# Kernel tuning notes

Measured on AMD Instinct MI355X. Metric: run time of the kernel, lower is better.

## Reference

```python
import jax, jax.numpy as jnp
import numpy as np

B, T, C, HD = 4, 4096, 1024, 64

def setup_inputs() -> dict:
    key = jax.random.key(0)
    k1, k2, k3, k4 = jax.random.split(key, 4)
    x = jax.random.normal(k1, (B, T, C), dtype=jnp.float32)
    scale = 1.0 / np.sqrt(C)
    Wq = jax.random.normal(k2, (C, HD), dtype=jnp.float32) * scale
    Wk = jax.random.normal(k3, (C, HD), dtype=jnp.float32) * scale
    Wv = jax.random.normal(k4, (C, HD), dtype=jnp.float32) * scale
    return {"x": x, "Wq": Wq, "Wk": Wk, "Wv": Wv}

def reference(x, Wq, Wk, Wv):
    # q,k,v: [B,T,HD]
    q = jnp.einsum('btc,ch->bth', x, Wq)
    k = jnp.einsum('btc,ch->bth', x, Wk)
    v = jnp.einsum('btc,ch->bth', x, Wv)
    hd = q.shape[-1]
    scores = jnp.einsum('bth,bsh->bts', q, k) / jnp.sqrt(jnp.float32(hd))  # [B,T,T]
    causal = jnp.tril(jnp.ones((scores.shape[1], scores.shape[1]), dtype=bool))
    scores = jnp.where(causal, scores, -jnp.inf)
    attn = jax.nn.softmax(scores, axis=-1)
    return jnp.einsum('bts,bsh->bth', attn, v)  # [B,T,HD]
```

## Files before the change

### kernel.cpp

```cpp
#include <hip/hip_runtime.h>
#include <hip/hip_bf16.h>

typedef __attribute__((ext_vector_type(8))) short bf16x8;
typedef __attribute__((ext_vector_type(4))) short bf16x4;
typedef __attribute__((ext_vector_type(4))) float f32x4;
typedef __attribute__((ext_vector_type(4))) int   i32x4;

#define C2LOG 0.18033688011112042f
#define THR_RAW 44.3616f

__device__ __forceinline__ short f2bf(float f) {
    union { float f; unsigned u; } v; v.f = f;
    unsigned r = v.u + 0x7fff + ((v.u >> 16) & 1);
    return (short)(r >> 16);
}
__device__ __forceinline__ unsigned cvtpk(float lo, float hi) {
    unsigned r;
    asm("v_cvt_pk_bf16_f32 %0, %1, %2" : "=v"(r) : "v"(lo), "v"(hi));
    return r;
}
__device__ __forceinline__ float bf2f(short s) {
    union { unsigned u; float f; } v; v.u = ((unsigned)(unsigned short)s) << 16;
    return v.f;
}
__device__ __forceinline__ float4 gload4(const float* p) {
    float4 r;
    asm volatile("global_load_dwordx4 %0, %1, off"
                 : "=&v"(r) : "v"(p) : "memory");
    return r;
}

#define BB 4
#define TT 4096
#define CC 1024
#define HD 64
#define NTASK_PB 144
#define NTASK (BB * NTASK_PB)

__global__ __launch_bounds__(256) void prep_w(const float* __restrict__ Wq,
        const float* __restrict__ Wk, const float* __restrict__ Wv,
        short* __restrict__ Wt) {
    __shared__ float wls[64][65];
    const int w = blockIdx.x >> 4;
    const int c = blockIdx.x & 15;
    const float* W = (w == 0) ? Wq : (w == 1) ? Wk : Wv;

    const int r  = threadIdx.x >> 4;
    const int q4 = threadIdx.x & 15;
    #pragma unroll
    for (int rr = 0; rr < 4; ++rr) {
        const int row = rr * 16 + r;
        float4 v = *reinterpret_cast<const float4*>(
            W + (size_t)(c * 64 + row) * HD + q4 * 4);
        wls[row][q4 * 4 + 0] = v.x;
        wls[row][q4 * 4 + 1] = v.y;
        wls[row][q4 * 4 + 2] = v.z;
        wls[row][q4 * 4 + 3] = v.w;
    }
    __syncthreads();

    const int n  = threadIdx.x >> 2;
    const int ks = (threadIdx.x & 3) * 16;
    bf16x8 o0, o1;
    #pragma unroll
    for (int j = 0; j < 8; ++j) o0[j] = f2bf(wls[ks + j][n]);
    #pragma unroll
    for (int j = 0; j < 8; ++j) o1[j] = f2bf(wls[ks + 8 + j][n]);
    short* dst = Wt + (size_t)(w * 64 + n) * CC + c * 64 + ks;
    *reinterpret_cast<bf16x8*>(dst)     = o0;
    *reinterpret_cast<bf16x8*>(dst + 8) = o1;
}

__global__ __launch_bounds__(512) void proj_qkv(const float* __restrict__ x,
        const short* __restrict__ Wt, short* __restrict__ Q,
        short* __restrict__ K, short* __restrict__ Vt) {
    __shared__ short xs[2][32 * 72];
    __shared__ short wsm[2][192 * 64];

    const int tid  = threadIdx.x;
    const int lane = tid & 63;
    const int wv   = tid >> 6;
    const int lm   = lane & 15;
    const int lg   = lane >> 4;
    const int mhalf = wv & 1;
    const int ngrp  = wv >> 1;
    const int mbase = blockIdx.x * 32;

    const int xr  = tid >> 4;
    const int xq4 = tid & 15;
    const float* xrow = x + (size_t)(mbase + xr) * CC;

    int wsrow[3], wscol[3];
    #pragma unroll
    for (int it = 0; it < 3; ++it) {
        const int off = it * 8192 + wv * 1024 + lane * 16;
        wsrow[it] = off >> 7;
        wscol[it] = (off & 127) ^ ((wsrow[it] & 7) << 4);
    }

#define STAGE_W(bufidx, kc)                                                           \
    {                                                                                 \
        _Pragma("unroll")                                                             \
        for (int it = 0; it < 3; ++it) {                                              \
            const char* src = (const char*)(Wt + (size_t)wsrow[it] * CC + (kc) * 64)  \
                              + wscol[it];                                            \
            char* dst = (char*)&wsm[bufidx][0] + it * 8192 + wv * 1024;               \
            __builtin_amdgcn_global_load_lds(                                         \
                (const __attribute__((address_space(1))) unsigned*)src,               \
                (__attribute__((address_space(3))) unsigned*)dst, 16, 0, 0);          \
        }                                                                             \
    }

#define CONV_X(bufidx, xv)                                                            \
    {                                                                                 \
        int2 pk;                                                                      \
        pk.x = (int)cvtpk((xv).x, (xv).y);                                            \
        pk.y = (int)cvtpk((xv).z, (xv).w);                                            \
        *reinterpret_cast<int2*>(&xs[bufidx][xr * 72 + xq4 * 4]) = pk;                \
    }

    f32x4 acc[3];
    #pragma unroll
    for (int i = 0; i < 3; ++i) acc[i] = f32x4{0.f, 0.f, 0.f, 0.f};

    {
        float4 v = *reinterpret_cast<const float4*>(xrow + xq4 * 4);
        CONV_X(0, v)
        STAGE_W(0, 0)
    }
    float4 vA = gload4(xrow + 64 + xq4 * 4);
    asm volatile("s_waitcnt vmcnt(1)" ::: "memory");
    asm volatile("s_waitcnt lgkmcnt(0)" ::: "memory");
    __builtin_amdgcn_s_barrier();

    const int arow = mhalf * 16 + lm;
    int buf = 0;
    for (int kc = 0; kc < 16; ++kc) {
        if (kc < 15) STAGE_W(buf ^ 1, kc + 1)
        float4 vB;
        if (kc < 14) vB = gload4(xrow + (kc + 2) * 64 + xq4 * 4);

        bf16x8 a0 = *reinterpret_cast<const bf16x8*>(&xs[buf][arow * 72 + lg * 8]);
        bf16x8 a1 = *reinterpret_cast<const bf16x8*>(&xs[buf][arow * 72 + 32 + lg * 8]);
        __builtin_amdgcn_s_setprio(1);
        #pragma unroll
        for (int c = 0; c < 3; ++c) {
            const int brow = (ngrp * 3 + c) * 16 + lm;
            const int sw = (brow & 7) << 4;
            bf16x8 b0 = *reinterpret_cast<const bf16x8*>(
                (const char*)&wsm[buf][0] + brow * 128 + ((lg * 16) ^ sw));
            bf16x8 b1 = *reinterpret_cast<const bf16x8*>(
                (const char*)&wsm[buf][0] + brow * 128 + ((64 + lg * 16) ^ sw));
            acc[c] = __builtin_amdgcn_mfma_f32_16x16x32_bf16(a0, b0, acc[c], 0, 0, 0);
            acc[c] = __builtin_amdgcn_mfma_f32_16x16x32_bf16(a1, b1, acc[c], 0, 0, 0);
        }
        __builtin_amdgcn_s_setprio(0);

        if (kc < 15) {
            if (kc < 14) asm volatile("s_waitcnt vmcnt(4)" ::: "memory");
            else         asm volatile("s_waitcnt vmcnt(3)" ::: "memory");
            __builtin_amdgcn_sched_barrier(0);
            CONV_X(buf ^ 1, vA)
        }
        vA = vB;

        if (kc < 15) {
            __builtin_amdgcn_sched_barrier(0);
            if (kc < 14) asm volatile("s_waitcnt vmcnt(1)" ::: "memory");
            else         asm volatile("s_waitcnt vmcnt(0)" ::: "memory");
            asm volatile("s_waitcnt lgkmcnt(0)" ::: "memory");
            __builtin_amdgcn_s_barrier();
        }
        buf ^= 1;
    }
#undef STAGE_W
#undef CONV_X

    const int mrow = mbase + mhalf * 16 + lg * 4;
    #pragma unroll
    for (int c = 0; c < 3; ++c) {
        const int cn = ngrp * 3 + c;
        if (cn < 4) {
            #pragma unroll
            for (int r = 0; r < 4; ++r)
                Q[(size_t)(mrow + r) * HD + cn * 16 + lm] = f2bf(acc[c][r]);
        } else if (cn < 8) {
            #pragma unroll
            for (int r = 0; r < 4; ++r)
                K[(size_t)(mrow + r) * HD + (cn - 4) * 16 + lm] = f2bf(acc[c][r]);
        } else {
            const int bb   = mbase >> 12;
            const int tloc = (mbase & 4095) + mhalf * 16 + lg * 4;
            int2 pk;
            pk.x = (int)cvtpk(acc[c][0], acc[c][1]);
            pk.y = (int)cvtpk(acc[c][2], acc[c][3]);
            *reinterpret_cast<int2*>(
                Vt + (size_t)bb * (HD * TT) + (size_t)((cn - 8) * 16 + lm) * TT + tloc) = pk;
        }
    }
}

__global__ __launch_bounds__(256, 3) void attn(const short* __restrict__ Q,
        const short* __restrict__ K, const short* __restrict__ Vt,
        short* __restrict__ Opart, float* __restrict__ Mpart,
        float* __restrict__ Lpart, float* __restrict__ out) {
    __shared__ short ks[3][64 * 64];
    __shared__ short vs[3][64 * 64];

    const int tid  = threadIdx.x;
    const int lane = tid & 63;
    const int wv   = tid >> 6;
    const int lm   = lane & 15;
    const int lg   = lane >> 4;

    const int task = (blockIdx.x & 7) * (NTASK / 8) + (blockIdx.x >> 3);
    const int b  = task / NTASK_PB;
    int t_in = task - b * NTASK_PB;
    int g = 0;
    while (t_in >= 2 * (g + 1) * (g + 2)) ++g;
    const int idx = t_in - 2 * g * (g + 1);
    const int i   = 4 * g + idx / (g + 1);
    const int seg = idx % (g + 1);
    const int S   = g + 1;
    const int niter = 2 * i + 2;
    const int nloop = (niter - seg + S - 1) / S;

    const size_t qkb = (size_t)b * TT * HD;
    const size_t vtb = (size_t)b * HD * TT;
    const int qrow = i * 128 + wv * 32;
    const int tmax = (qrow + 31) >> 6;

    bf16x8 qf0 = *reinterpret_cast<const bf16x8*>(Q + qkb + (size_t)(qrow + lm) * HD + lg * 8);
    bf16x8 qf1 = *reinterpret_cast<const bf16x8*>(Q + qkb + (size_t)(qrow + lm) * HD + 32 + lg * 8);
    bf16x8 qf2 = *reinterpret_cast<const bf16x8*>(Q + qkb + (size_t)(qrow + 16 + lm) * HD + lg * 8);
    bf16x8 qf3 = *reinterpret_cast<const bf16x8*>(Q + qkb + (size_t)(qrow + 16 + lm) * HD + 32 + lg * 8);

    f32x4 oA[4], oB[4];
    #pragma unroll
    for (int c = 0; c < 4; ++c) { oA[c] = f32x4{0.f,0.f,0.f,0.f}; oB[c] = f32x4{0.f,0.f,0.f,0.f}; }
    float mrunA = -1e30f, lrunA = 0.f;
    float mrunB = -1e30f, lrunB = 0.f;

    const int srcA = lm + ((lane & 16) << 1);
    const int srcB = srcA + 16;
    const bool hihalf = (lane & 32) != 0;

    int srow[2], scol[2];
    #pragma unroll
    for (int c = 0; c < 2; ++c) {
        const int off = wv * 2048 + c * 1024 + lane * 16;
        srow[c] = off >> 7;
        scol[c] = (off & 127) ^ ((srow[c] & 7) << 4);
    }

#define STAGE_KV(bufidx, tt)                                                          \
    {                                                                                 \
        _Pragma("unroll")                                                             \
        for (int c = 0; c < 2; ++c) {                                                 \
            const char* ksrc = (const char*)(K + qkb) + (tt) * 8192                   \
                               + (srow[c] << 7) + scol[c];                            \
            char* kdst = (char*)&ks[bufidx][0] + wv * 2048 + c * 1024;                \
            __builtin_amdgcn_global_load_lds(                                         \
                (const __attribute__((address_space(1))) unsigned*)ksrc,              \
                (__attribute__((address_space(3))) unsigned*)kdst, 16, 0, 0);         \
            const char* vsrc = (const char*)(Vt + vtb) + (size_t)srow[c] * (TT * 2)   \
                               + (tt) * 128 + scol[c];                                \
            char* vdst = (char*)&vs[bufidx][0] + wv * 2048 + c * 1024;                \
            __builtin_amdgcn_global_load_lds(                                         \
                (const __attribute__((address_space(1))) unsigned*)vsrc,              \
                (__attribute__((address_space(3))) unsigned*)vdst, 16, 0, 0);         \
        }                                                                             \
    }

    STAGE_KV(0, seg)
    if (nloop > 1) {
        STAGE_KV(1, seg + S)
        asm volatile("s_waitcnt vmcnt(4)" ::: "memory");
    } else {
        asm volatile("s_waitcnt vmcnt(0)" ::: "memory");
    }
    __builtin_amdgcn_s_barrier();

    for (int n = 0; n < nloop; ++n) {
        const int t = seg + n * S;
        const bool stage2 = (n + 2 < nloop);
        if (stage2) STAGE_KV((n + 2) % 3, t + 2 * S)

        if (t <= tmax) {
            const short* ksb = &ks[n % 3][0];
            const short* vsb = &vs[n % 3][0];
            const int kv = t * 64;

            f32x4 stA[4], stB[4];
            __builtin_amdgcn_s_setprio(1);
            #pragma unroll
            for (int kt = 0; kt < 4; ++kt) {
                const int krow = kt * 16 + lm;
                const int sw = (krow & 7) << 4;
                bf16x8 k0 = *reinterpret_cast<const bf16x8*>(
                    (const char*)ksb + krow * 128 + ((lg * 16) ^ sw));
                bf16x8 k1 = *reinterpret_cast<const bf16x8*>(
                    (const char*)ksb + krow * 128 + ((64 + lg * 16) ^ sw));
                f32x4 a = f32x4{0.f,0.f,0.f,0.f};
                a = __builtin_amdgcn_mfma_f32_16x16x32_bf16(k0, qf0, a, 0, 0, 0);
                a = __builtin_amdgcn_mfma_f32_16x16x32_bf16(k1, qf1, a, 0, 0, 0);
                stA[kt] = a;
                f32x4 bb2 = f32x4{0.f,0.f,0.f,0.f};
                bb2 = __builtin_amdgcn_mfma_f32_16x16x32_bf16(k0, qf2, bb2, 0, 0, 0);
                bb2 = __builtin_amdgcn_mfma_f32_16x16x32_bf16(k1, qf3, bb2, 0, 0, 0);
                stB[kt] = bb2;
            }
            __builtin_amdgcn_s_setprio(0);

            if (kv + 63 > qrow) {
                const int qgA = qrow + lm;
                const int qgB = qrow + 16 + lm;
                #pragma unroll
                for (int kt = 0; kt < 4; ++kt)
                    #pragma unroll
                    for (int r = 0; r < 4; ++r) {
                        const int kk = kv + kt * 16 + lg * 4 + r;
                        if (kk > qgA) stA[kt][r] = -1e30f;
                        if (kk > qgB) stB[kt][r] = -1e30f;
                    }
            }

            float mA0 = fmaxf(fmaxf(stA[0][0], stA[0][1]), fmaxf(stA[0][2], stA[0][3]));
            float mA1 = fmaxf(fmaxf(stA[1][0], stA[1][1]), fmaxf(stA[1][2], stA[1][3]));
            float mA2 = fmaxf(fmaxf(stA[2][0], stA[2][1]), fmaxf(stA[2][2], stA[2][3]));
            float mA3 = fmaxf(fmaxf(stA[3][0], stA[3][1]), fmaxf(stA[3][2], stA[3][3]));
            float mlocA = fmaxf(fmaxf(mA0, mA1), fmaxf(mA2, mA3));
            float mB0 = fmaxf(fmaxf(stB[0][0], stB[0][1]), fmaxf(stB[0][2], stB[0][3]));
            float mB1 = fmaxf(fmaxf(stB[1][0], stB[1][1]), fmaxf(stB[1][2], stB[1][3]));
            float mB2 = fmaxf(fmaxf(stB[2][0], stB[2][1]), fmaxf(stB[2][2], stB[2][3]));
            float mB3 = fmaxf(fmaxf(stB[3][0], stB[3][1]), fmaxf(stB[3][2], stB[3][3]));
            float mlocB = fmaxf(fmaxf(mB0, mB1), fmaxf(mB2, mB3));
            mlocA = fmaxf(mlocA, __shfl_xor(mlocA, 16));
            mlocA = fmaxf(mlocA, __shfl_xor(mlocA, 32));
            mlocB = fmaxf(mlocB, __shfl_xor(mlocB, 16));
            mlocB = fmaxf(mlocB, __shfl_xor(mlocB, 32));

            if (!__all(mlocA <= mrunA + THR_RAW)) {
                const float mnewA = fmaxf(mrunA, mlocA);
                const float alphaA = __builtin_amdgcn_exp2f((mrunA - mnewA) * C2LOG);
                mrunA = mnewA;
                lrunA *= alphaA;
                #pragma unroll
                for (int c = 0; c < 4; ++c)
                    #pragma unroll
                    for (int r = 0; r < 4; ++r) oA[c][r] *= alphaA;
            }
            if (!__all(mlocB <= mrunB + THR_RAW)) {
                const float mnewB = fmaxf(mrunB, mlocB);
                const float alphaB = __builtin_amdgcn_exp2f((mrunB - mnewB) * C2LOG);
                mrunB = mnewB;
                lrunB *= alphaB;
                #pragma unroll
                for (int c = 0; c < 4; ++c)
                    #pragma unroll
                    for (int r = 0; r < 4; ++r) oB[c][r] *= alphaB;
            }

            const float ncA = -mrunA * C2LOG;
            const float ncB = -mrunB * C2LOG;
            float pA[4][4], pB[4][4];
            float rsA = 0.f, rsB = 0.f;
            #pragma unroll
            for (int kt = 0; kt < 4; ++kt)
                #pragma unroll
                for (int r = 0; r < 4; ++r) {
                    pA[kt][r] = __builtin_amdgcn_exp2f(__builtin_fmaf(stA[kt][r], C2LOG, ncA));
                    rsA += pA[kt][r];
                    pB[kt][r] = __builtin_amdgcn_exp2f(__builtin_fmaf(stB[kt][r], C2LOG, ncB));
                    rsB += pB[kt][r];
                }
            rsA += __shfl_xor(rsA, 16); rsA += __shfl_xor(rsA, 32);
            rsB += __shfl_xor(rsB, 16); rsB += __shfl_xor(rsB, 32);
            lrunA += rsA;
            lrunB += rsB;

            unsigned uA[4][2], uB[4][2];
            #pragma unroll
            for (int kt = 0; kt < 4; ++kt) {
                uA[kt][0] = cvtpk(pA[kt][0], pA[kt][1]);
                uA[kt][1] = cvtpk(pA[kt][2], pA[kt][3]);
                uB[kt][0] = cvtpk(pB[kt][0], pB[kt][1]);
                uB[kt][1] = cvtpk(pB[kt][2], pB[kt][3]);
            }

            #pragma unroll
            for (int h = 0; h < 2; ++h) {
                const int a0 = __shfl((int)uA[2*h][0],   srcA);
                const int a1c = __shfl((int)uA[2*h+1][0], srcA);
                const int a2 = __shfl((int)uA[2*h][1],   srcA);
                const int a3c = __shfl((int)uA[2*h+1][1], srcA);
                const int a4 = __shfl((int)uA[2*h][0],   srcB);
                const int a5c = __shfl((int)uA[2*h+1][0], srcB);
                const int a6 = __shfl((int)uA[2*h][1],   srcB);
                const int a7c = __shfl((int)uA[2*h+1][1], srcB);
                union { i32x4 iv; bf16x8 v; } cvA;
                cvA.iv = i32x4{ hihalf ? a1c : a0, hihalf ? a3c : a2,
                                hihalf ? a5c : a4, hihalf ? a7c : a6 };
                const int b0 = __shfl((int)uB[2*h][0],   srcA);
                const int b1c = __shfl((int)uB[2*h+1][0], srcA);
                const int b2 = __shfl((int)uB[2*h][1],   srcA);
                const int b3c = __shfl((int)uB[2*h+1][1], srcA);
                const int b4 = __shfl((int)uB[2*h][0],   srcB);
                const int b5c = __shfl((int)uB[2*h+1][0], srcB);
                const int b6 = __shfl((int)uB[2*h][1],   srcB);
                const int b7c = __shfl((int)uB[2*h+1][1], srcB);
                union { i32x4 iv; bf16x8 v; } cvB;
                cvB.iv = i32x4{ hihalf ? b1c : b0, hihalf ? b3c : b2,
                                hihalf ? b5c : b4, hihalf ? b7c : b6 };
                __builtin_amdgcn_s_setprio(1);
                #pragma unroll
                for (int c = 0; c < 4; ++c) {
                    const int vrow = c * 16 + lm;
                    const int sw = (vrow & 7) << 4;
                    bf16x8 va = *reinterpret_cast<const bf16x8*>(
                        (const char*)vsb + vrow * 128 + ((h * 64 + lg * 16) ^ sw));
                    oA[c] = __builtin_amdgcn_mfma_f32_16x16x32_bf16(va, cvA.v, oA[c], 0, 0, 0);
                    oB[c] = __builtin_amdgcn_mfma_f32_16x16x32_bf16(va, cvB.v, oB[c], 0, 0, 0);
                }
                __builtin_amdgcn_s_setprio(0);
            }
        }

        __builtin_amdgcn_sched_barrier(0);
        asm volatile("s_waitcnt lgkmcnt(0)" ::: "memory");
        if (stage2) asm volatile("s_waitcnt vmcnt(4)" ::: "memory");
        else        asm volatile("s_waitcnt vmcnt(0)" ::: "memory");
        __builtin_amdgcn_s_barrier();
    }
#undef STAGE_KV

    if (S == 1) {
        const float invA = 1.0f / lrunA;
        const float invB = 1.0f / lrunB;
        float* Orow = out + ((size_t)b * TT + i * 128) * HD;
        #pragma unroll
        for (int c = 0; c < 4; ++c) {
            f32x4 ra, rb;
            #pragma unroll
            for (int r = 0; r < 4; ++r) { ra[r] = oA[c][r] * invA; rb[r] = oB[c][r] * invB; }
            *reinterpret_cast<f32x4*>(&Orow[(size_t)(wv * 32 + lm) * HD + c * 16 + lg * 4]) = ra;
            *reinterpret_cast<f32x4*>(&Orow[(size_t)(wv * 32 + 16 + lm) * HD + c * 16 + lg * 4]) = rb;
        }
        return;
    }

    short* Ob = Opart + (size_t)task * (128 * HD);
    #pragma unroll
    for (int c = 0; c < 4; ++c) {
        int2 pkA, pkB;
        pkA.x = (int)cvtpk(oA[c][0], oA[c][1]);
        pkA.y = (int)cvtpk(oA[c][2], oA[c][3]);
        pkB.x = (int)cvtpk(oB[c][0], oB[c][1]);
        pkB.y = (int)cvtpk(oB[c][2], oB[c][3]);
        *reinterpret_cast<int2*>(&Ob[(wv * 32 + lm) * HD + c * 16 + lg * 4]) = pkA;
        *reinterpret_cast<int2*>(&Ob[(wv * 32 + 16 + lm) * HD + c * 16 + lg * 4]) = pkB;
    }
    if (lg == 0) {
        Mpart[task * 128 + wv * 32 + lm] = mrunA;
        Lpart[task * 128 + wv * 32 + lm] = lrunA;
        Mpart[task * 128 + wv * 32 + 16 + lm] = mrunB;
        Lpart[task * 128 + wv * 32 + 16 + lm] = lrunB;
    }
}

__global__ __launch_bounds__(256) void combine(const short* __restrict__ Opart,
        const float* __restrict__ Mpart, const float* __restrict__ Lpart,
        float* __restrict__ out) {
    const int b   = blockIdx.x / 224;
    const int rem = blockIdx.x - b * 224;
    const int i   = 4 + (rem >> 3);
    const int rr  = rem & 7;
    const int g = i >> 2;
    const int S = g + 1;
    const int task0 = b * NTASK_PB + 2 * g * (g + 1) + (i - 4 * g) * (g + 1);
    const int qbase = i * 128;

    const int tid = threadIdx.x;
    const int row = rr * 16 + (tid >> 4);
    const int cb  = (tid & 15) << 2;

    float mmax = -1e30f;
    float ms[8];
    for (int s = 0; s < S; ++s) {
        ms[s] = Mpart[(task0 + s) * 128 + row];
        mmax = fmaxf(mmax, ms[s]);
    }
    float lsum = 0.f;
    float a0 = 0.f, a1 = 0.f, a2 = 0.f, a3 = 0.f;
    for (int s = 0; s < S; ++s) {
        const float w = __builtin_amdgcn_exp2f((ms[s] - mmax) * C2LOG);
        lsum += Lpart[(task0 + s) * 128 + row] * w;
        bf16x4 ov = *reinterpret_cast<const bf16x4*>(
            &Opart[((size_t)(task0 + s) * 128 + row) * HD + cb]);
        a0 += bf2f(ov[0]) * w;
        a1 += bf2f(ov[1]) * w;
        a2 += bf2f(ov[2]) * w;
        a3 += bf2f(ov[3]) * w;
    }
    const float inv = 1.0f / lsum;
    f32x4 res{ a0 * inv, a1 * inv, a2 * inv, a3 * inv };
    *reinterpret_cast<f32x4*>(
        &out[((size_t)b * TT + qbase + row) * HD + cb]) = res;
}

extern "C" void kernel_launch(void* const* d_in, const int* in_sizes, int n_in,
                              void* d_out, int out_size, void* d_ws, size_t ws_size,
                              hipStream_t stream) {
    const float* x  = (const float*)d_in[0];
    const float* Wq = (const float*)d_in[1];
    const float* Wk = (const float*)d_in[2];
    const float* Wv = (const float*)d_in[3];
    float* out = (float*)d_out;

    char* ws = (char*)d_ws;
    short* Wt    = (short*)(ws);
    short* Q     = (short*)(ws + 393216);
    short* K     = (short*)(ws + 2490368);
    short* Vt    = (short*)(ws + 4587520);
    short* Opart = (short*)(ws + 6684672);
    float* Mpart = (float*)(ws + 16121856);
    float* Lpart = (float*)(ws + 16416768);

    hipLaunchKernelGGL(prep_w,   dim3(48),    dim3(256), 0, stream, Wq, Wk, Wv, Wt);
    hipLaunchKernelGGL(proj_qkv, dim3(512),   dim3(512), 0, stream, x, Wt, Q, K, Vt);
    hipLaunchKernelGGL(attn,     dim3(NTASK), dim3(256), 0, stream, Q, K, Vt,
                       Opart, Mpart, Lpart, out);
    hipLaunchKernelGGL(combine,  dim3(896),   dim3(256), 0, stream,
                       Opart, Mpart, Lpart, out);
}
```

Baseline: 61.41 us.

## Split attention block into 8 waves with 16 query rows each

The attention kernel now launches 512 threads (8 waves) per block, and each wave handles 16 query rows instead of 32. Every wave stages one 16-byte chunk of K and V per tile instead of two. This halves per-wave register state (accumulators, scores, probabilities), which should raise occupancy and latency hiding. The cost is that each K/V fragment read from LDS now feeds half as many MFMAs, so LDS traffic per FLOP doubles, and barrier synchronization now spans more waves. The launch bound claims 6 blocks of 512 threads, which may not fit on the hardware and could force heavy register limits.

New measurement: 61.47 us. No clear change (+0.1%).

```diff
diff --git a/kernel.cpp b/kernel.cpp
--- a/kernel.cpp
+++ b/kernel.cpp
@@ -200,7 +200,7 @@
     }
 }
 
-__global__ __launch_bounds__(256, 3) void attn(const short* __restrict__ Q,
+__global__ __launch_bounds__(512, 6) void attn(const short* __restrict__ Q,
         const short* __restrict__ K, const short* __restrict__ Vt,
         short* __restrict__ Opart, float* __restrict__ Mpart,
         float* __restrict__ Lpart, float* __restrict__ out) {
@@ -227,55 +227,44 @@
 
     const size_t qkb = (size_t)b * TT * HD;
     const size_t vtb = (size_t)b * HD * TT;
-    const int qrow = i * 128 + wv * 32;
-    const int tmax = (qrow + 31) >> 6;
+    const int qrow = i * 128 + wv * 16;
+    const int tmax = (qrow + 15) >> 6;
 
     bf16x8 qf0 = *reinterpret_cast<const bf16x8*>(Q + qkb + (size_t)(qrow + lm) * HD + lg * 8);
     bf16x8 qf1 = *reinterpret_cast<const bf16x8*>(Q + qkb + (size_t)(qrow + lm) * HD + 32 + lg * 8);
-    bf16x8 qf2 = *reinterpret_cast<const bf16x8*>(Q + qkb + (size_t)(qrow + 16 + lm) * HD + lg * 8);
-    bf16x8 qf3 = *reinterpret_cast<const bf16x8*>(Q + qkb + (size_t)(qrow + 16 + lm) * HD + 32 + lg * 8);
-
-    f32x4 oA[4], oB[4];
-    #pragma unroll
-    for (int c = 0; c < 4; ++c) { oA[c] = f32x4{0.f,0.f,0.f,0.f}; oB[c] = f32x4{0.f,0.f,0.f,0.f}; }
-    float mrunA = -1e30f, lrunA = 0.f;
-    float mrunB = -1e30f, lrunB = 0.f;
+
+    f32x4 o[4];
+    #pragma unroll
+    for (int c = 0; c < 4; ++c) o[c] = f32x4{0.f,0.f,0.f,0.f};
+    float mrun = -1e30f, lrun = 0.f;
 
     const int srcA = lm + ((lane & 16) << 1);
     const int srcB = srcA + 16;
     const bool hihalf = (lane & 32) != 0;
 
-    int srow[2], scol[2];
-    #pragma unroll
-    for (int c = 0; c < 2; ++c) {
-        const int off = wv * 2048 + c * 1024 + lane * 16;
-        srow[c] = off >> 7;
-        scol[c] = (off & 127) ^ ((srow[c] & 7) << 4);
-    }
+    const int soff = wv * 1024 + lane * 16;
+    const int srow = soff >> 7;
+    const int scol = (soff & 127) ^ ((srow & 7) << 4);
 
 #define STAGE_KV(bufidx, tt)                                                          \
     {                                                                                 \
-        _Pragma("unroll")                                                             \
-        for (int c = 0; c < 2; ++c) {                                                 \
-            const char* ksrc = (const char*)(K + qkb) + (tt) * 8192                   \
-                               + (srow[c] << 7) + scol[c];                            \
-            char* kdst = (char*)&ks[bufidx][0] + wv * 2048 + c * 1024;                \
-            __builtin_amdgcn_global_load_lds(                                         \
-                (const __attribute__((address_space(1))) unsigned*)ksrc,              \
-                (__attribute__((address_space(3))) unsigned*)kdst, 16, 0, 0);         \
-            const char* vsrc = (const char*)(Vt + vtb) + (size_t)srow[c] * (TT * 2)   \
-                               + (tt) * 128 + scol[c];                                \
-            char* vdst = (char*)&vs[bufidx][0] + wv * 2048 + c * 1024;                \
-            __builtin_amdgcn_global_load_lds(                                         \
-                (const __attribute__((address_space(1))) unsigned*)vsrc,              \
-                (__attribute__((address_space(3))) unsigned*)vdst, 16, 0, 0);         \
-        }                                                                             \
+        const char* ksrc = (const char*)(K + qkb) + (tt) * 8192 + (srow << 7) + scol; \
+        char* kdst = (char*)&ks[bufidx][0] + wv * 1024;                               \
+        __builtin_amdgcn_global_load_lds(                                             \
+            (const __attribute__((address_space(1))) unsigned*)ksrc,                  \
+            (__attribute__((address_space(3))) unsigned*)kdst, 16, 0, 0);             \
+        const char* vsrc = (const char*)(Vt + vtb) + (size_t)srow * (TT * 2)          \
+                           + (tt) * 128 + scol;                                       \
+        char* vdst = (char*)&vs[bufidx][0] + wv * 1024;                               \
+        __builtin_amdgcn_global_load_lds(                                             \
+            (const __attribute__((address_space(1))) unsigned*)vsrc,                  \
+            (__attribute__((address_space(3))) unsigned*)vdst, 16, 0, 0);             \
     }
 
     STAGE_KV(0, seg)
     if (nloop > 1) {
         STAGE_KV(1, seg + S)
-        asm volatile("s_waitcnt vmcnt(4)" ::: "memory");
+        asm volatile("s_waitcnt vmcnt(2)" ::: "memory");
     } else {
         asm volatile("s_waitcnt vmcnt(0)" ::: "memory");
     }
@@ -291,7 +280,7 @@
             const short* vsb = &vs[n % 3][0];
             const int kv = t * 64;
 
-            f32x4 stA[4], stB[4];
+            f32x4 st[4];
             __builtin_amdgcn_s_setprio(1);
             #pragma unroll
             for (int kt = 0; kt < 4; ++kt) {
@@ -304,114 +293,72 @@
                 f32x4 a = f32x4{0.f,0.f,0.f,0.f};
                 a = __builtin_amdgcn_mfma_f32_16x16x32_bf16(k0, qf0, a, 0, 0, 0);
                 a = __builtin_amdgcn_mfma_f32_16x16x32_bf16(k1, qf1, a, 0, 0, 0);
-                stA[kt] = a;
-                f32x4 bb2 = f32x4{0.f,0.f,0.f,0.f};
-                bb2 = __builtin_amdgcn_mfma_f32_16x16x32_bf16(k0, qf2, bb2, 0, 0, 0);
-                bb2 = __builtin_amdgcn_mfma_f32_16x16x32_bf16(k1, qf3, bb2, 0, 0, 0);
-                stB[kt] = bb2;
+                st[kt] = a;
             }
             __builtin_amdgcn_s_setprio(0);
 
             if (kv + 63 > qrow) {
-                const int qgA = qrow + lm;
-                const int qgB = qrow + 16 + lm;
+                const int qg = qrow + lm;
                 #pragma unroll
                 for (int kt = 0; kt < 4; ++kt)
                     #pragma unroll
-                    for (int r = 0; r < 4; ++r) {
-                        const int kk = kv + kt * 16 + lg * 4 + r;
-                        if (kk > qgA) stA[kt][r] = -1e30f;
-                        if (kk > qgB) stB[kt][r] = -1e30f;
-                    }
+                    for (int r = 0; r < 4; ++r)
+                        if (kv + kt * 16 + lg * 4 + r > qg) st[kt][r] = -1e30f;
             }
 
-            float mA0 = fmaxf(fmaxf(stA[0][0], stA[0][1]), fmaxf(stA[0][2], stA[0][3]));
-            float mA1 = fmaxf(fmaxf(stA[1][0], stA[1][1]), fmaxf(stA[1][2], stA[1][3]));
-            float mA2 = fmaxf(fmaxf(stA[2][0], stA[2][1]), fmaxf(stA[2][2], stA[2][3]));
-            float mA3 = fmaxf(fmaxf(stA[3][0], stA[3][1]), fmaxf(stA[3][2], stA[3][3]));
-            float mlocA = fmaxf(fmaxf(mA0, mA1), fmaxf(mA2, mA3));
-            float mB0 = fmaxf(fmaxf(stB[0][0], stB[0][1]), fmaxf(stB[0][2], stB[0][3]));
-            float mB1 = fmaxf(fmaxf(stB[1][0], stB[1][1]), fmaxf(stB[1][2], stB[1][3]));
-            float mB2 = fmaxf(fmaxf(stB[2][0], stB[2][1]), fmaxf(stB[2][2], stB[2][3]));
-            float mB3 = fmaxf(fmaxf(stB[3][0], stB[3][1]), fmaxf(stB[3][2], stB[3][3]));
-            float mlocB = fmaxf(fmaxf(mB0, mB1), fmaxf(mB2, mB3));
-            mlocA = fmaxf(mlocA, __shfl_xor(mlocA, 16));
-            mlocA = fmaxf(mlocA, __shfl_xor(mlocA, 32));
-            mlocB = fmaxf(mlocB, __shfl_xor(mlocB, 16));
-            mlocB = fmaxf(mlocB, __shfl_xor(mlocB, 32));
-
-            if (!__all(mlocA <= mrunA + THR_RAW)) {
-                const float mnewA = fmaxf(mrunA, mlocA);
-                const float alphaA = __builtin_amdgcn_exp2f((mrunA - mnewA) * C2LOG);
-                mrunA = mnewA;
-                lrunA *= alphaA;
+            float m0 = fmaxf(fmaxf(st[0][0], st[0][1]), fmaxf(st[0][2], st[0][3]));
+            float m1 = fmaxf(fmaxf(st[1][0], st[1][1]), fmaxf(st[1][2], st[1][3]));
+            float m2 = fmaxf(fmaxf(st[2][0], st[2][1]), fmaxf(st[2][2], st[2][3]));
+            float m3 = fmaxf(fmaxf(st[3][0], st[3][1]), fmaxf(st[3][2], st[3][3]));
+            float mloc = fmaxf(fmaxf(m0, m1), fmaxf(m2, m3));
+            mloc = fmaxf(mloc, __shfl_xor(mloc, 16));
+            mloc = fmaxf(mloc, __shfl_xor(mloc, 32));
+
+            if (!__all(mloc <= mrun + THR_RAW)) {
+                const float mnew = fmaxf(mrun, mloc);
+                const float alpha = __builtin_amdgcn_exp2f((mrun - mnew) * C2LOG);
+                mrun = mnew;
+                lrun *= alpha;
                 #pragma unroll
                 for (int c = 0; c < 4; ++c)
                     #pragma unroll
-                    for (int r = 0; r < 4; ++r) oA[c][r] *= alphaA;
+                    for (int r = 0; r < 4; ++r) o[c][r] *= alpha;
             }
-            if (!__all(mlocB <= mrunB + THR_RAW)) {
-                const float mnewB = fmaxf(mrunB, mlocB);
-                const float alphaB = __builtin_amdgcn_exp2f((mrunB - mnewB) * C2LOG);
-                mrunB = mnewB;
-                lrunB *= alphaB;
-                #pragma unroll
-                for (int c = 0; c < 4; ++c)
-                    #pragma unroll
-                    for (int r = 0; r < 4; ++r) oB[c][r] *= alphaB;
-            }
-
-            const float ncA = -mrunA * C2LOG;
-            const float ncB = -mrunB * C2LOG;
-            float pA[4][4], pB[4][4];
-            float rsA = 0.f, rsB = 0.f;
+
+            const float nc = -mrun * C2LOG;
+            float p[4][4];
+            float rs = 0.f;
             #pragma unroll
             for (int kt = 0; kt < 4; ++kt)
                 #pragma unroll
                 for (int r = 0; r < 4; ++r) {
-                    pA[kt][r] = __builtin_amdgcn_exp2f(__builtin_fmaf(stA[kt][r], C2LOG, ncA));
-                    rsA += pA[kt][r];
-                    pB[kt][r] = __builtin_amdgcn_exp2f(__builtin_fmaf(stB[kt][r], C2LOG, ncB));
-                    rsB += pB[kt][r];
+                    p[kt][r] = __builtin_amdgcn_exp2f(__builtin_fmaf(st[kt][r], C2LOG, nc));
+                    rs += p[kt][r];
                 }
-            rsA += __shfl_xor(rsA, 16); rsA += __shfl_xor(rsA, 32);
-            rsB += __shfl_xor(rsB, 16); rsB += __shfl_xor(rsB, 32);
-            lrunA += rsA;
-            lrunB += rsB;
-
-            unsigned uA[4][2], uB[4][2];
+            rs += __shfl_xor(rs, 16);
+            rs += __shfl_xor(rs, 32);
+            lrun += rs;
+
+            unsigned u[4][2];
             #pragma unroll
             for (int kt = 0; kt < 4; ++kt) {
-                uA[kt][0] = cvtpk(pA[kt][0], pA[kt][1]);
-                uA[kt][1] = cvtpk(pA[kt][2], pA[kt][3]);
-                uB[kt][0] = cvtpk(pB[kt][0], pB[kt][1]);
-                uB[kt][1] = cvtpk(pB[kt][2], pB[kt][3]);
+                u[kt][0] = cvtpk(p[kt][0], p[kt][1]);
+                u[kt][1] = cvtpk(p[kt][2], p[kt][3]);
             }
 
             #pragma unroll
             for (int h = 0; h < 2; ++h) {
-                const int a0 = __shfl((int)uA[2*h][0],   srcA);
-                const int a1c = __shfl((int)uA[2*h+1][0], srcA);
-                const int a2 = __shfl((int)uA[2*h][1],   srcA);
-                const int a3c = __shfl((int)uA[2*h+1][1], srcA);
-                const int a4 = __shfl((int)uA[2*h][0],   srcB);
-                const int a5c = __shfl((int)uA[2*h+1][0], srcB);
-                const int a6 = __shfl((int)uA[2*h][1],   srcB);
-                const int a7c = __shfl((int)uA[2*h+1][1], srcB);
-                union { i32x4 iv; bf16x8 v; } cvA;
-                cvA.iv = i32x4{ hihalf ? a1c : a0, hihalf ? a3c : a2,
-                                hihalf ? a5c : a4, hihalf ? a7c : a6 };
-                const int b0 = __shfl((int)uB[2*h][0],   srcA);
-                const int b1c = __shfl((int)uB[2*h+1][0], srcA);
-                const int b2 = __shfl((int)uB[2*h][1],   srcA);
-                const int b3c = __shfl((int)uB[2*h+1][1], srcA);
-                const int b4 = __shfl((int)uB[2*h][0],   srcB);
-                const int b5c = __shfl((int)uB[2*h+1][0], srcB);
-                const int b6 = __shfl((int)uB[2*h][1],   srcB);
-                const int b7c = __shfl((int)uB[2*h+1][1], srcB);
-                union { i32x4 iv; bf16x8 v; } cvB;
-                cvB.iv = i32x4{ hihalf ? b1c : b0, hihalf ? b3c : b2,
-                                hihalf ? b5c : b4, hihalf ? b7c : b6 };
+                const int b0 = __shfl((int)u[2*h][0],   srcA);
+                const int c0 = __shfl((int)u[2*h+1][0], srcA);
+                const int b1 = __shfl((int)u[2*h][1],   srcA);
+                const int c1 = __shfl((int)u[2*h+1][1], srcA);
+                const int b2 = __shfl((int)u[2*h][0],   srcB);
+                const int c2 = __shfl((int)u[2*h+1][0], srcB);
+                const int b3 = __shfl((int)u[2*h][1],   srcB);
+                const int c3 = __shfl((int)u[2*h+1][1], srcB);
+                union { i32x4 iv; bf16x8 v; } cv;
+                cv.iv = i32x4{ hihalf ? c0 : b0, hihalf ? c1 : b1,
+                               hihalf ? c2 : b2, hihalf ? c3 : b3 };
                 __builtin_amdgcn_s_setprio(1);
                 #pragma unroll
                 for (int c = 0; c < 4; ++c) {
@@ -419,8 +366,7 @@
                     const int sw = (vrow & 7) << 4;
                     bf16x8 va = *reinterpret_cast<const bf16x8*>(
                         (const char*)vsb + vrow * 128 + ((h * 64 + lg * 16) ^ sw));
-                    oA[c] = __builtin_amdgcn_mfma_f32_16x16x32_bf16(va, cvA.v, oA[c], 0, 0, 0);
-                    oB[c] = __builtin_amdgcn_mfma_f32_16x16x32_bf16(va, cvB.v, oB[c], 0, 0, 0);
+                    o[c] = __builtin_amdgcn_mfma_f32_16x16x32_bf16(va, cv.v, o[c], 0, 0, 0);
                 }
                 __builtin_amdgcn_s_setprio(0);
             }
@@ -428,23 +374,22 @@
 
         __builtin_amdgcn_sched_barrier(0);
         asm volatile("s_waitcnt lgkmcnt(0)" ::: "memory");
-        if (stage2) asm volatile("s_waitcnt vmcnt(4)" ::: "memory");
+        if (stage2) asm volatile("s_waitcnt vmcnt(2)" ::: "memory");
         else        asm volatile("s_waitcnt vmcnt(0)" ::: "memory");
         __builtin_amdgcn_s_barrier();
     }
 #undef STAGE_KV
 
     if (S == 1) {
-        const float invA = 1.0f / lrunA;
-        const float invB = 1.0f / lrunB;
+        const float inv = 1.0f / lrun;
         float* Orow = out + ((size_t)b * TT + i * 128) * HD;
         #pragma unroll
         for (int c = 0; c < 4; ++c) {
-            f32x4 ra, rb;
-            #pragma unroll
-            for (int r = 0; r < 4; ++r) { ra[r] = oA[c][r] * invA; rb[r] = oB[c][r] * invB; }
-            *reinterpret_cast<f32x4*>(&Orow[(size_t)(wv * 32 + lm) * HD + c * 16 + lg * 4]) = ra;
-            *reinterpret_cast<f32x4*>(&Orow[(size_t)(wv * 32 + 16 + lm) * HD + c * 16 + lg * 4]) = rb;
+            f32x4 ra;
+            #pragma unroll
+            for (int r = 0; r < 4; ++r) ra[r] = o[c][r] * inv;
+            *reinterpret_cast<f32x4*>(
+                &Orow[(size_t)(wv * 16 + lm) * HD + c * 16 + lg * 4]) = ra;
         }
         return;
     }
@@ -452,19 +397,14 @@
     short* Ob = Opart + (size_t)task * (128 * HD);
     #pragma unroll
     for (int c = 0; c < 4; ++c) {
-        int2 pkA, pkB;
-        pkA.x = (int)cvtpk(oA[c][0], oA[c][1]);
-        pkA.y = (int)cvtpk(oA[c][2], oA[c][3]);
-        pkB.x = (int)cvtpk(oB[c][0], oB[c][1]);
-        pkB.y = (int)cvtpk(oB[c][2], oB[c][3]);
-        *reinterpret_cast<int2*>(&Ob[(wv * 32 + lm) * HD + c * 16 + lg * 4]) = pkA;
-        *reinterpret_cast<int2*>(&Ob[(wv * 32 + 16 + lm) * HD + c * 16 + lg * 4]) = pkB;
+        int2 pk;
+        pk.x = (int)cvtpk(o[c][0], o[c][1]);
+        pk.y = (int)cvtpk(o[c][2], o[c][3]);
+        *reinterpret_cast<int2*>(&Ob[(wv * 16 + lm) * HD + c * 16 + lg * 4]) = pk;
     }
     if (lg == 0) {
-        Mpart[task * 128 + wv * 32 + lm] = mrunA;
-        Lpart[task * 128 + wv * 32 + lm] = lrunA;
-        Mpart[task * 128 + wv * 32 + 16 + lm] = mrunB;
-        Lpart[task * 128 + wv * 32 + 16 + lm] = lrunB;
+        Mpart[task * 128 + wv * 16 + lm] = mrun;
+        Lpart[task * 128 + wv * 16 + lm] = lrun;
     }
 }
 
@@ -528,7 +468,7 @@
 
     hipLaunchKernelGGL(prep_w,   dim3(48),    dim3(256), 0, stream, Wq, Wk, Wv, Wt);
     hipLaunchKernelGGL(proj_qkv, dim3(512),   dim3(512), 0, stream, x, Wt, Q, K, Vt);
-    hipLaunchKernelGGL(attn,     dim3(NTASK), dim3(256), 0, stream, Q, K, Vt,
+    hipLaunchKernelGGL(attn,     dim3(NTASK), dim3(512), 0, stream, Q, K, Vt,
                        Opart, Mpart, Lpart, out);
     hipLaunchKernelGGL(combine,  dim3(896),   dim3(256), 0, stream,
                        Opart, Mpart, Lpart, out);
```
